# Kernel optimization log

Hardware: AMD Instinct MI355X
Metric: run time of the kernel (lower is better)

## Reference

```python
import jax, jax.numpy as jnp
import numpy as np

N = 100000      # nodes
E = 1600000     # edges (avg degree 16)
D_IN, D_H, D_OUT = 128, 128, 64


def _pow(d, e):
    # torch code zeroes out inf from 0 ** negative_exponent
    p = jnp.power(d, e)
    return jnp.where(jnp.isinf(p), jnp.zeros_like(p), p)


def _gso_weights(params, deg, row, col):
    # params = [m1, m2, m3, e1, e2, e3, a]
    m1, m2, m3, e1, e2, e3, a = (params[i] for i in range(7))
    d = deg + a                       # self-loop-adjusted degrees, [N]
    pe2 = _pow(d, e2)
    pe3 = _pow(d, e3)
    w_edge = m2 * pe2[row] * pe3[col]                     # off-diagonal GSO entries, [E]
    w_self = m1 * _pow(d, e1) + m2 * pe2 * pe3 + m3       # diagonal GSO entries, [N]
    return w_edge, w_self


def setup_inputs() -> dict:
    key = jax.random.key(0)
    ks = jax.random.split(key, 8)
    x = jax.random.normal(ks[0], (N, D_IN), dtype=jnp.float32)
    edge_index = jax.random.randint(ks[1], (2, E), 0, N, dtype=jnp.int32)
    glorot = lambda k, i, o: jax.random.normal(k, (i, o), dtype=jnp.float32) * np.float32(np.sqrt(2.0 / (i + o)))
    W1 = glorot(ks[2], D_IN, D_H)
    W2 = glorot(ks[3], D_H, D_H)
    W3 = glorot(ks[4], D_H, D_OUT)
    b1 = jnp.zeros((D_H,), jnp.float32)
    b2 = jnp.zeros((D_H,), jnp.float32)
    b3 = jnp.zeros((D_OUT,), jnp.float32)
    # [m1, m2, m3, e1, e2, e3, a]
    gso1_params = jnp.array([0.0, 1.0, 0.0, 0.0, -0.5, -0.5, 1.0], jnp.float32)   # NORMADJ
    gso2_params = jnp.array([0.0, -1.0, 1.0, 0.0, -1.0, 0.0, 0.0], jnp.float32)   # RWLAPLACIAN
    return {"x": x, "edge_index": edge_index, "W1": W1, "b1": b1, "W2": W2,
            "b2": b2, "W3": W3, "b3": b3, "gso1_params": gso1_params,
            "gso2_params": gso2_params}


def reference(x, edge_index, W1, b1, W2, b2, W3, b3, gso1_params, gso2_params):
    row, col = edge_index[0], edge_index[1]
    deg = jax.ops.segment_sum(jnp.ones(row.shape, x.dtype), row, num_segments=N)
    we1, ws1 = _gso_weights(gso1_params, deg, row, col)
    we2, ws2 = _gso_weights(gso2_params, deg, row, col)
    w_edge = we1 + we2   # combined two-GSO edge weights, [E]
    w_self = ws1 + ws2   # combined diagonal (self-loop) weights, [N]

    def conv(h, W, b):
        h = h @ W                                                        # [N, d_out]
        agg = jax.ops.segment_sum(w_edge[:, None] * h[col], row, num_segments=N)
        return agg + w_self[:, None] * h + b

    h = jax.nn.relu(conv(x, W1, b1))
    h = jax.nn.relu(conv(h, W2, b2))   # dropout=0.0 (eval) -> identity
    return conv(h, W3, b3)
```

## Files before the change

### kernel.cpp

```cpp
#include <hip/hip_runtime.h>
#include <hip/hip_fp16.h>
#include <math.h>
#include <type_traits>

typedef _Float16 half8 __attribute__((ext_vector_type(8)));
typedef float floatx4 __attribute__((ext_vector_type(4)));

#define RSHIFT 9
#define AGG_BLOCKS 2048

__global__ __launch_bounds__(256) void hist_conv_kernel(
        const int* __restrict__ row, int E, int* __restrict__ bucketsize,
        const float* __restrict__ W1, const float* __restrict__ W2,
        const float* __restrict__ W3, _Float16* __restrict__ Wt1,
        _Float16* __restrict__ Wt2, _Float16* __restrict__ Wt3, int histBlocks) {
    int tid = threadIdx.x;
    if ((int)blockIdx.x < histBlocks) {
        __shared__ int h[256];
        h[tid] = 0;
        __syncthreads();
        int base = blockIdx.x * 16384;
#pragma unroll
        for (int it = 0; it < 16; ++it) {
            int e0 = base + it * 1024 + tid * 4;
            if (e0 + 3 < E) {
                int4 r4 = *(const int4*)&row[e0];
                atomicAdd(&h[r4.x >> RSHIFT], 1);
                atomicAdd(&h[r4.y >> RSHIFT], 1);
                atomicAdd(&h[r4.z >> RSHIFT], 1);
                atomicAdd(&h[r4.w >> RSHIFT], 1);
            } else {
#pragma unroll
                for (int j = 0; j < 4; ++j)
                    if (e0 + j < E) atomicAdd(&h[row[e0 + j] >> RSHIFT], 1);
            }
        }
        __syncthreads();
        if (h[tid]) atomicAdd(&bucketsize[tid], h[tid]);
    } else {
        int g = ((int)blockIdx.x - histBlocks) * 256 + tid;
        if (g < 16384) {
            int k = g >> 7, n = g & 127;
            Wt1[n * 128 + k] = (_Float16)W1[g];
        } else if (g < 32768) {
            int h2 = g - 16384; int k = h2 >> 7, n = h2 & 127;
            Wt2[n * 128 + k] = (_Float16)W2[h2];
        } else if (g < 40960) {
            int h2 = g - 32768; int k = h2 >> 6, n = h2 & 63;
            Wt3[n * 128 + k] = (_Float16)W3[h2];
        }
    }
}

__global__ void scan_buckets_kernel(const int* __restrict__ bucketsize,
                                    int* __restrict__ bucketbase,
                                    int* __restrict__ rowptr, int N, int E) {
    __shared__ int s[256];
    int tid = threadIdx.x;
    int v = bucketsize[tid];
    s[tid] = v;
    __syncthreads();
    for (int off = 1; off < 256; off <<= 1) {
        int u = (tid >= off) ? s[tid - off] : 0;
        __syncthreads();
        s[tid] += u;
        __syncthreads();
    }
    bucketbase[tid] = s[tid] - v;
    if (tid == 255) bucketbase[256] = s[255];
    if (tid == 0) rowptr[N] = E;
}

__global__ __launch_bounds__(256) void partition_kernel(
        const int* __restrict__ row, const int* __restrict__ col,
        const int* __restrict__ bucketbase, int* __restrict__ gcur,
        int* __restrict__ emid, int E, int NB) {
    __shared__ int scnt[256], sofs[256], gslot[256];
    __shared__ int sdata[4096];
    __shared__ unsigned short sbkt[4096];

    int tid = threadIdx.x;
    int base = blockIdx.x * 4096;
    scnt[tid] = 0;
    __syncthreads();

    int epk[16]; int eb[16]; int eidx[16];
#pragma unroll
    for (int v = 0; v < 4; ++v) {
        int e0 = base + v * 1024 + tid * 4;
        int4 r4, c4;
        bool full = (e0 + 3 < E);
        if (full) {
            r4 = *(const int4*)&row[e0];
            c4 = *(const int4*)&col[e0];
        }
#pragma unroll
        for (int j = 0; j < 4; ++j) {
            int u = v * 4 + j;
            eb[u] = -1;
            int r, c;
            if (full) {
                r = (&r4.x)[j]; c = (&c4.x)[j];
            } else {
                if (e0 + j >= E) continue;
                r = row[e0 + j]; c = col[e0 + j];
            }
            int b = r >> RSHIFT;
            eb[u] = b;
            eidx[u] = atomicAdd(&scnt[b], 1);
            epk[u] = c | ((r & ((1 << RSHIFT) - 1)) << 20);
        }
    }
    __syncthreads();
    sofs[tid] = scnt[tid];
    __syncthreads();
    for (int off = 1; off < 256; off <<= 1) {
        int v = (tid >= off) ? sofs[tid - off] : 0;
        __syncthreads();
        sofs[tid] += v;
        __syncthreads();
    }
    int excl = sofs[tid] - scnt[tid];
    sofs[tid] = excl;
    if (tid < NB && scnt[tid] > 0)
        gslot[tid] = bucketbase[tid] + atomicAdd(&gcur[tid], scnt[tid]);
    __syncthreads();
#pragma unroll
    for (int u = 0; u < 16; ++u) {
        if (eb[u] >= 0) {
            int idx = sofs[eb[u]] + eidx[u];
            sdata[idx] = epk[u];
            sbkt[idx] = (unsigned short)eb[u];
        }
    }
    __syncthreads();
    int cntR = min(4096, E - base);
    for (int i = tid; i < cntR; i += 256) {
        int b = sbkt[i];
        emid[gslot[b] + (i - sofs[b])] = sdata[i];
    }
}

__device__ __forceinline__ float pow_z(float d, float e) {
    float p = powf(d, e);
    return isinf(p) ? 0.0f : p;
}

__device__ __forceinline__ void gso_coeff(float deg, const float* __restrict__ p1,
                                          const float* __restrict__ p2,
                                          float4* cf, float* ws) {
    float m1a = p1[0], m2a = p1[1], m3a = p1[2], e1a = p1[3], e2a = p1[4], e3a = p1[5], aa = p1[6];
    float m1b = p2[0], m2b = p2[1], m3b = p2[2], e1b = p2[3], e2b = p2[4], e3b = p2[5], ab = p2[6];
    float d1 = deg + aa, d2 = deg + ab;
    float pa1 = pow_z(d1, e1a), pa2 = pow_z(d1, e2a), pa3 = pow_z(d1, e3a);
    float pb1 = pow_z(d2, e1b), pb2 = pow_z(d2, e2b), pb3 = pow_z(d2, e3b);
    *cf = make_float4(m2a * pa2, pa3, m2b * pb2, pb3);
    *ws = m1a * pa1 + m2a * pa2 * pa3 + m3a
        + m1b * pb1 + m2b * pb2 * pb3 + m3b;
}

__global__ __launch_bounds__(256) void bucket_deg_kernel(
        const int* __restrict__ bucketbase, const int* __restrict__ emid,
        int* __restrict__ rowptr,
        const float* __restrict__ p1, const float* __restrict__ p2,
        float4* __restrict__ coeff, float* __restrict__ wself, int N) {
    __shared__ int cnt[512];
    __shared__ int ssum[256];
    int b = blockIdx.x;
    int tid = threadIdx.x;
    int row0 = b << RSHIFT;
    int nrows = min(512, N - row0);
    cnt[tid] = 0; cnt[tid + 256] = 0;
    __syncthreads();
    int seg0 = bucketbase[b], seg1 = bucketbase[b + 1];
    for (int i = seg0 + tid; i < seg1; i += 256)
        atomicAdd(&cnt[((unsigned)emid[i]) >> 20], 1);
    __syncthreads();
    int a0 = cnt[2 * tid], a1 = cnt[2 * tid + 1];
    int tsum = a0 + a1;
    ssum[tid] = tsum;
    __syncthreads();
    for (int off = 1; off < 256; off <<= 1) {
        int v = (tid >= off) ? ssum[tid - off] : 0;
        __syncthreads();
        ssum[tid] += v;
        __syncthreads();
    }
    int excl = ssum[tid] - tsum;
    if (2 * tid < nrows) {
        rowptr[row0 + 2 * tid] = seg0 + excl;
        float4 cf; float ws;
        gso_coeff((float)a0, p1, p2, &cf, &ws);
        coeff[row0 + 2 * tid] = cf;
        wself[row0 + 2 * tid] = ws;
    }
    if (2 * tid + 1 < nrows) {
        rowptr[row0 + 2 * tid + 1] = seg0 + excl + a0;
        float4 cf; float ws;
        gso_coeff((float)a1, p1, p2, &cf, &ws);
        coeff[row0 + 2 * tid + 1] = cf;
        wself[row0 + 2 * tid + 1] = ws;
    }
}

__global__ __launch_bounds__(256) void bucket_place_kernel(
        const int* __restrict__ bucketbase, const int* __restrict__ emid,
        const int* __restrict__ rowptr, const float4* __restrict__ coeff,
        int2* __restrict__ epack, int N) {
    __shared__ int lcur[512];
    __shared__ float4 scoef[512];
    int b = blockIdx.x;
    int tid = threadIdx.x;
    int row0 = b << RSHIFT;
    int nrows = min(512, N - row0);
#pragma unroll
    for (int u = 0; u < 2; ++u) {
        int j = tid + u * 256;
        if (j < nrows) {
            lcur[j] = rowptr[row0 + j];
            scoef[j] = coeff[row0 + j];
        }
    }
    __syncthreads();
    int seg0 = bucketbase[b], seg1 = bucketbase[b + 1];
    for (int i = seg0 + tid; i < seg1; i += 256) {
        int v = emid[i];
        int rl = ((unsigned)v) >> 20;
        int c = v & 0xFFFFF;
        float4 cr = scoef[rl];
        float4 cc = coeff[c];
        float w = cr.x * cc.y + cr.z * cc.w;
        int pos = atomicAdd(&lcur[rl], 1);
        epack[pos] = make_int2(c, __float_as_int(w));
    }
}

template<int TN, typename AT>
__global__ __launch_bounds__(256) void gemm_mfma(const AT* __restrict__ A,
        const _Float16* __restrict__ Wt, _Float16* __restrict__ C, int n) {
    constexpr int K = 128;
    constexpr int TM = 128;
    constexpr int LDK = K + 8;
    __shared__ _Float16 As[TM][LDK];
    __shared__ _Float16 Bs[TN][LDK];

    int tid = threadIdx.x;
    int wave = tid >> 6, lane = tid & 63;
    int q = lane >> 4, t = lane & 15;
    int rowbase = blockIdx.x * TM;

    if constexpr (std::is_same<AT, float>::value) {
        for (int i = tid; i < TM * K / 4; i += 256) {
            int r = i >> 5;
            int kc = (i & 31) * 4;
            int rr = rowbase + r;
            float4 v = make_float4(0.f, 0.f, 0.f, 0.f);
            if (rr < n) v = *(const float4*)&A[(size_t)rr * K + kc];
            As[r][kc + 0] = (_Float16)v.x;
            As[r][kc + 1] = (_Float16)v.y;
            As[r][kc + 2] = (_Float16)v.z;
            As[r][kc + 3] = (_Float16)v.w;
        }
    } else {
        for (int i = tid; i < TM * K / 8; i += 256) {
            int r = i >> 4;
            int kc = (i & 15) * 8;
            int rr = rowbase + r;
            uint4 v = make_uint4(0u, 0u, 0u, 0u);
            if (rr < n) v = *(const uint4*)&A[(size_t)rr * K + kc];
            *(uint4*)&As[r][kc] = v;
        }
    }
    for (int i = tid; i < TN * K / 8; i += 256) {
        int nr = i >> 4;
        int kc = (i & 15) * 8;
        *(uint4*)&Bs[nr][kc] = *(const uint4*)&Wt[(size_t)nr * K + kc];
    }
    __syncthreads();

    int m0 = wave * 32;
    floatx4 acc0[TN / 16], acc1[TN / 16];
#pragma unroll
    for (int nt = 0; nt < TN / 16; ++nt) {
        acc0[nt] = (floatx4){0.f, 0.f, 0.f, 0.f};
        acc1[nt] = (floatx4){0.f, 0.f, 0.f, 0.f};
    }

#pragma unroll
    for (int kk = 0; kk < K; kk += 32) {
        half8 a0 = *(const half8*)&As[m0 + t][kk + q * 8];
        half8 a1 = *(const half8*)&As[m0 + 16 + t][kk + q * 8];
#pragma unroll
        for (int nt = 0; nt < TN / 16; ++nt) {
            half8 b = *(const half8*)&Bs[nt * 16 + t][kk + q * 8];
            acc0[nt] = __builtin_amdgcn_mfma_f32_16x16x32_f16(a0, b, acc0[nt], 0, 0, 0);
            acc1[nt] = __builtin_amdgcn_mfma_f32_16x16x32_f16(a1, b, acc1[nt], 0, 0, 0);
        }
    }

#pragma unroll
    for (int nt = 0; nt < TN / 16; ++nt) {
#pragma unroll
        for (int r = 0; r < 4; ++r) {
            int rr0 = rowbase + m0 + q * 4 + r;
            if (rr0 < n) C[(size_t)rr0 * TN + nt * 16 + t] = (_Float16)acc0[nt][r];
            int rr1 = rr0 + 16;
            if (rr1 < n) C[(size_t)rr1 * TN + nt * 16 + t] = (_Float16)acc1[nt][r];
        }
    }
}

__global__ __launch_bounds__(256) void agg128_kernel(const __half2* __restrict__ H,
        const int* __restrict__ rowptr, const int2* __restrict__ epack,
        const float* __restrict__ wself, const float* __restrict__ bias,
        __half2* __restrict__ out, int n) {
    int wid = blockIdx.x * 4 + (threadIdx.x >> 6);
    int nw = gridDim.x * 4;
    int lane = threadIdx.x & 63;
    float2 b = *(const float2*)&bias[2 * lane];
    for (int node = wid; node < n; node += nw) {
        int start = rowptr[node], end = rowptr[node + 1];
        float ws = wself[node];
        float2 hs = __half22float2(H[(size_t)node * 64 + lane]);
        float ax = ws * hs.x, ay = ws * hs.y;
        int e = start;
        for (; e + 16 <= end; e += 16) {
            int2 p[16];
#pragma unroll
            for (int j = 0; j < 16; ++j) p[j] = epack[e + j];
            __half2 hh[16];
#pragma unroll
            for (int j = 0; j < 16; ++j) hh[j] = H[(size_t)p[j].x * 64 + lane];
#pragma unroll
            for (int j = 0; j < 16; ++j) {
                float w = __int_as_float(p[j].y);
                float2 f = __half22float2(hh[j]);
                ax += w * f.x; ay += w * f.y;
            }
        }
        if (e + 8 <= end) {
            int2 p[8];
#pragma unroll
            for (int j = 0; j < 8; ++j) p[j] = epack[e + j];
            __half2 hh[8];
#pragma unroll
            for (int j = 0; j < 8; ++j) hh[j] = H[(size_t)p[j].x * 64 + lane];
#pragma unroll
            for (int j = 0; j < 8; ++j) {
                float w = __int_as_float(p[j].y);
                float2 f = __half22float2(hh[j]);
                ax += w * f.x; ay += w * f.y;
            }
            e += 8;
        }
        if (e + 4 <= end) {
            int2 p[4];
#pragma unroll
            for (int j = 0; j < 4; ++j) p[j] = epack[e + j];
            __half2 hh[4];
#pragma unroll
            for (int j = 0; j < 4; ++j) hh[j] = H[(size_t)p[j].x * 64 + lane];
#pragma unroll
            for (int j = 0; j < 4; ++j) {
                float w = __int_as_float(p[j].y);
                float2 f = __half22float2(hh[j]);
                ax += w * f.x; ay += w * f.y;
            }
            e += 4;
        }
        for (; e < end; ++e) {
            int2 pe = epack[e];
            float w = __int_as_float(pe.y);
            float2 f = __half22float2(H[(size_t)pe.x * 64 + lane]);
            ax += w * f.x; ay += w * f.y;
        }
        float vx = fmaxf(ax + b.x, 0.0f);
        float vy = fmaxf(ay + b.y, 0.0f);
        out[(size_t)node * 64 + lane] = __floats2half2_rn(vx, vy);
    }
}

__global__ __launch_bounds__(256) void agg64_kernel(const __half* __restrict__ H,
        const int* __restrict__ rowptr, const int2* __restrict__ epack,
        const float* __restrict__ wself, const float* __restrict__ bias,
        float* __restrict__ out, int n) {
    int wid = blockIdx.x * 4 + (threadIdx.x >> 6);
    int nw = gridDim.x * 4;
    int lane = threadIdx.x & 63;
    float b = bias[lane];
    for (int node = wid; node < n; node += nw) {
        int start = rowptr[node], end = rowptr[node + 1];
        float ws = wself[node];
        float acc = ws * __half2float(H[(size_t)node * 64 + lane]);
        int e = start;
        for (; e + 16 <= end; e += 16) {
            int2 p[16];
#pragma unroll
            for (int j = 0; j < 16; ++j) p[j] = epack[e + j];
            float f[16];
#pragma unroll
            for (int j = 0; j < 16; ++j) f[j] = __half2float(H[(size_t)p[j].x * 64 + lane]);
#pragma unroll
            for (int j = 0; j < 16; ++j) acc += __int_as_float(p[j].y) * f[j];
        }
        if (e + 8 <= end) {
            int2 p[8];
#pragma unroll
            for (int j = 0; j < 8; ++j) p[j] = epack[e + j];
            float f[8];
#pragma unroll
            for (int j = 0; j < 8; ++j) f[j] = __half2float(H[(size_t)p[j].x * 64 + lane]);
#pragma unroll
            for (int j = 0; j < 8; ++j) acc += __int_as_float(p[j].y) * f[j];
            e += 8;
        }
        if (e + 4 <= end) {
            int2 p[4];
#pragma unroll
            for (int j = 0; j < 4; ++j) p[j] = epack[e + j];
            float f[4];
#pragma unroll
            for (int j = 0; j < 4; ++j) f[j] = __half2float(H[(size_t)p[j].x * 64 + lane]);
#pragma unroll
            for (int j = 0; j < 4; ++j) acc += __int_as_float(p[j].y) * f[j];
            e += 4;
        }
        for (; e < end; ++e) {
            int2 pe = epack[e];
            acc += __int_as_float(pe.y) * __half2float(H[(size_t)pe.x * 64 + lane]);
        }
        out[(size_t)node * 64 + lane] = acc + b;
    }
}

extern "C" void kernel_launch(void* const* d_in, const int* in_sizes, int n_in,
                              void* d_out, int out_size, void* d_ws, size_t ws_size,
                              hipStream_t stream) {
    const float* x  = (const float*)d_in[0];
    const int*   ei = (const int*)d_in[1];
    const float* W1 = (const float*)d_in[2];
    const float* b1 = (const float*)d_in[3];
    const float* W2 = (const float*)d_in[4];
    const float* b2 = (const float*)d_in[5];
    const float* W3 = (const float*)d_in[6];
    const float* b3 = (const float*)d_in[7];
    const float* p1 = (const float*)d_in[8];
    const float* p2 = (const float*)d_in[9];

    const int N = in_sizes[0] / 128;
    const int E = in_sizes[1] / 2;
    const int* row = ei;
    const int* col = ei + E;
    const int NB = ((N - 1) >> RSHIFT) + 1;

    char* p = (char*)d_ws;
    auto alloc = [&](size_t bytes) -> void* {
        void* q = (void*)p;
        p += (bytes + 255) & ~(size_t)255;
        return q;
    };
    int*      bucketsize = (int*)alloc(256 * 4);
    int*      gcur       = (int*)alloc(256 * 4);
    int*      bucketbase = (int*)alloc(257 * 4);
    int*      rowptr     = (int*)alloc((size_t)(N + 1) * 4);
    float4*   coeff      = (float4*)alloc((size_t)N * 16);
    float*    wself      = (float*)alloc((size_t)N * 4);
    int*      emid       = (int*)alloc((size_t)E * 4);
    int2*     epack      = (int2*)alloc((size_t)E * 8);
    _Float16* Wt1        = (_Float16*)alloc(128 * 128 * 2);
    _Float16* Wt2        = (_Float16*)alloc(128 * 128 * 2);
    _Float16* Wt3        = (_Float16*)alloc(128 * 64 * 2);
    _Float16* bufH       = (_Float16*)alloc((size_t)N * 128 * 2);
    _Float16* actH       = (_Float16*)alloc((size_t)N * 128 * 2);
    (void)ws_size; (void)n_in;

    hipMemsetAsync(bucketsize, 0, 512 * 4, stream);

    const int histBlocks = (E + 16383) / 16384;
    const int convBlocks = (40960 + 255) / 256;
    hist_conv_kernel<<<histBlocks + convBlocks, 256, 0, stream>>>(
        row, E, bucketsize, W1, W2, W3, Wt1, Wt2, Wt3, histBlocks);
    scan_buckets_kernel<<<1, 256, 0, stream>>>(bucketsize, bucketbase, rowptr, N, E);
    partition_kernel<<<(E + 4095) / 4096, 256, 0, stream>>>(row, col, bucketbase, gcur,
                                                            emid, E, NB);
    bucket_deg_kernel<<<NB, 256, 0, stream>>>(bucketbase, emid, rowptr, p1, p2,
                                              coeff, wself, N);
    bucket_place_kernel<<<NB, 256, 0, stream>>>(bucketbase, emid, rowptr, coeff, epack, N);

    float* out = (float*)d_out;
    int gemmGrid = (N + 127) / 128;
    gemm_mfma<128, float><<<gemmGrid, 256, 0, stream>>>(x, Wt1, bufH, N);
    agg128_kernel<<<AGG_BLOCKS, 256, 0, stream>>>((const __half2*)bufH, rowptr, epack, wself,
                                                  b1, (__half2*)actH, N);
    gemm_mfma<128, _Float16><<<gemmGrid, 256, 0, stream>>>(actH, Wt2, bufH, N);
    agg128_kernel<<<AGG_BLOCKS, 256, 0, stream>>>((const __half2*)bufH, rowptr, epack, wself,
                                                  b2, (__half2*)actH, N);
    gemm_mfma<64, _Float16><<<gemmGrid, 256, 0, stream>>>(actH, Wt3, bufH, N);
    agg64_kernel<<<AGG_BLOCKS, 256, 0, stream>>>((const __half*)bufH, rowptr, epack, wself,
                                                 b3, out, N);
}
```

Baseline: 449.8 us.

## Fold bucket scan into consumer kernels and launch one wavefront per node in aggregation

```diff
diff --git a/kernel.cpp b/kernel.cpp
--- a/kernel.cpp
+++ b/kernel.cpp
@@ -7,7 +7,6 @@
 typedef float floatx4 __attribute__((ext_vector_type(4)));
 
 #define RSHIFT 9
-#define AGG_BLOCKS 2048
 
 __global__ __launch_bounds__(256) void hist_conv_kernel(
         const int* __restrict__ row, int E, int* __restrict__ bucketsize,
@@ -52,38 +51,40 @@
     }
 }
 
-__global__ void scan_buckets_kernel(const int* __restrict__ bucketsize,
-                                    int* __restrict__ bucketbase,
-                                    int* __restrict__ rowptr, int N, int E) {
-    __shared__ int s[256];
-    int tid = threadIdx.x;
-    int v = bucketsize[tid];
-    s[tid] = v;
+__device__ __forceinline__ void scan_bucketsize(const int* __restrict__ bucketsize,
+                                                int* s_incl, int* s_val) {
+    int tid = threadIdx.x & 255;
+    if (threadIdx.x < 256) {
+        int v = bucketsize[tid];
+        s_val[tid] = v;
+        s_incl[tid] = v;
+    }
     __syncthreads();
     for (int off = 1; off < 256; off <<= 1) {
-        int u = (tid >= off) ? s[tid - off] : 0;
-        __syncthreads();
-        s[tid] += u;
-        __syncthreads();
-    }
-    bucketbase[tid] = s[tid] - v;
-    if (tid == 255) bucketbase[256] = s[255];
-    if (tid == 0) rowptr[N] = E;
+        int v = 0;
+        if (threadIdx.x < 256 && tid >= off) v = s_incl[tid - off];
+        __syncthreads();
+        if (threadIdx.x < 256) s_incl[tid] += v;
+        __syncthreads();
+    }
 }
 
 __global__ __launch_bounds__(256) void partition_kernel(
         const int* __restrict__ row, const int* __restrict__ col,
-        const int* __restrict__ bucketbase, int* __restrict__ gcur,
+        const int* __restrict__ bucketsize, int* __restrict__ gcur,
         int* __restrict__ emid, int E, int NB) {
+    __shared__ int sincl[256], sval[256];
     __shared__ int scnt[256], sofs[256], gslot[256];
     __shared__ int sdata[4096];
     __shared__ unsigned short sbkt[4096];
 
     int tid = threadIdx.x;
+    scan_bucketsize(bucketsize, sincl, sval);
+    int mybase = sincl[tid] - sval[tid];
+    scnt[tid] = 0;
+    __syncthreads();
+
     int base = blockIdx.x * 4096;
-    scnt[tid] = 0;
-    __syncthreads();
-
     int epk[16]; int eb[16]; int eidx[16];
 #pragma unroll
     for (int v = 0; v < 4; ++v) {
@@ -123,7 +124,7 @@
     int excl = sofs[tid] - scnt[tid];
     sofs[tid] = excl;
     if (tid < NB && scnt[tid] > 0)
-        gslot[tid] = bucketbase[tid] + atomicAdd(&gcur[tid], scnt[tid]);
+        gslot[tid] = mybase + atomicAdd(&gcur[tid], scnt[tid]);
     __syncthreads();
 #pragma unroll
     for (int u = 0; u < 16; ++u) {
@@ -160,19 +161,22 @@
 }
 
 __global__ __launch_bounds__(256) void bucket_deg_kernel(
-        const int* __restrict__ bucketbase, const int* __restrict__ emid,
+        const int* __restrict__ bucketsize, const int* __restrict__ emid,
         int* __restrict__ rowptr,
         const float* __restrict__ p1, const float* __restrict__ p2,
-        float4* __restrict__ coeff, float* __restrict__ wself, int N) {
+        float4* __restrict__ coeff, float* __restrict__ wself, int N, int NB) {
+    __shared__ int sincl[256], sval[256];
     __shared__ int cnt[512];
     __shared__ int ssum[256];
     int b = blockIdx.x;
     int tid = threadIdx.x;
+    scan_bucketsize(bucketsize, sincl, sval);
+    int seg0 = sincl[b] - sval[b];
+    int seg1 = sincl[b];
     int row0 = b << RSHIFT;
     int nrows = min(512, N - row0);
     cnt[tid] = 0; cnt[tid + 256] = 0;
     __syncthreads();
-    int seg0 = bucketbase[b], seg1 = bucketbase[b + 1];
     for (int i = seg0 + tid; i < seg1; i += 256)
         atomicAdd(&cnt[((unsigned)emid[i]) >> 20], 1);
     __syncthreads();
@@ -201,16 +205,21 @@
         coeff[row0 + 2 * tid + 1] = cf;
         wself[row0 + 2 * tid + 1] = ws;
     }
+    if (tid == 0 && b == NB - 1) rowptr[N] = seg1;
 }
 
 __global__ __launch_bounds__(256) void bucket_place_kernel(
-        const int* __restrict__ bucketbase, const int* __restrict__ emid,
+        const int* __restrict__ bucketsize, const int* __restrict__ emid,
         const int* __restrict__ rowptr, const float4* __restrict__ coeff,
         int2* __restrict__ epack, int N) {
+    __shared__ int sincl[256], sval[256];
     __shared__ int lcur[512];
     __shared__ float4 scoef[512];
     int b = blockIdx.x;
     int tid = threadIdx.x;
+    scan_bucketsize(bucketsize, sincl, sval);
+    int seg0 = sincl[b] - sval[b];
+    int seg1 = sincl[b];
     int row0 = b << RSHIFT;
     int nrows = min(512, N - row0);
 #pragma unroll
@@ -222,7 +231,6 @@
         }
     }
     __syncthreads();
-    int seg0 = bucketbase[b], seg1 = bucketbase[b + 1];
     for (int i = seg0 + tid; i < seg1; i += 256) {
         int v = emid[i];
         int rl = ((unsigned)v) >> 20;
@@ -310,127 +318,122 @@
     }
 }
 
-__global__ __launch_bounds__(256) void agg128_kernel(const __half2* __restrict__ H,
+__global__ __launch_bounds__(1024) void agg128_kernel(const __half2* __restrict__ H,
         const int* __restrict__ rowptr, const int2* __restrict__ epack,
         const float* __restrict__ wself, const float* __restrict__ bias,
         __half2* __restrict__ out, int n) {
-    int wid = blockIdx.x * 4 + (threadIdx.x >> 6);
-    int nw = gridDim.x * 4;
+    int node = blockIdx.x * 16 + (threadIdx.x >> 6);
+    if (node >= n) return;
     int lane = threadIdx.x & 63;
+    int start = rowptr[node], end = rowptr[node + 1];
+    float ws = wself[node];
+    float2 hs = __half22float2(H[(size_t)node * 64 + lane]);
+    float ax = ws * hs.x, ay = ws * hs.y;
+    int e = start;
+    for (; e + 16 <= end; e += 16) {
+        int2 p[16];
+#pragma unroll
+        for (int j = 0; j < 16; ++j) p[j] = epack[e + j];
+        __half2 hh[16];
+#pragma unroll
+        for (int j = 0; j < 16; ++j) hh[j] = H[(size_t)p[j].x * 64 + lane];
+#pragma unroll
+        for (int j = 0; j < 16; ++j) {
+            float w = __int_as_float(p[j].y);
+            float2 f = __half22float2(hh[j]);
+            ax += w * f.x; ay += w * f.y;
+        }
+    }
+    if (e + 8 <= end) {
+        int2 p[8];
+#pragma unroll
+        for (int j = 0; j < 8; ++j) p[j] = epack[e + j];
+        __half2 hh[8];
+#pragma unroll
+        for (int j = 0; j < 8; ++j) hh[j] = H[(size_t)p[j].x * 64 + lane];
+#pragma unroll
+        for (int j = 0; j < 8; ++j) {
+            float w = __int_as_float(p[j].y);
+            float2 f = __half22float2(hh[j]);
+            ax += w * f.x; ay += w * f.y;
+        }
+        e += 8;
+    }
+    if (e + 4 <= end) {
+        int2 p[4];
+#pragma unroll
+        for (int j = 0; j < 4; ++j) p[j] = epack[e + j];
+        __half2 hh[4];
+#pragma unroll
+        for (int j = 0; j < 4; ++j) hh[j] = H[(size_t)p[j].x * 64 + lane];
+#pragma unroll
+        for (int j = 0; j < 4; ++j) {
+            float w = __int_as_float(p[j].y);
+            float2 f = __half22float2(hh[j]);
+            ax += w * f.x; ay += w * f.y;
+        }
+        e += 4;
+    }
+    for (; e < end; ++e) {
+        int2 pe = epack[e];
+        float w = __int_as_float(pe.y);
+        float2 f = __half22float2(H[(size_t)pe.x * 64 + lane]);
+        ax += w * f.x; ay += w * f.y;
+    }
     float2 b = *(const float2*)&bias[2 * lane];
-    for (int node = wid; node < n; node += nw) {
-        int start = rowptr[node], end = rowptr[node + 1];
-        float ws = wself[node];
-        float2 hs = __half22float2(H[(size_t)node * 64 + lane]);
-        float ax = ws * hs.x, ay = ws * hs.y;
-        int e = start;
-        for (; e + 16 <= end; e += 16) {
-            int2 p[16];
-#pragma unroll
-            for (int j = 0; j < 16; ++j) p[j] = epack[e + j];
-            __half2 hh[16];
-#pragma unroll
-            for (int j = 0; j < 16; ++j) hh[j] = H[(size_t)p[j].x * 64 + lane];
-#pragma unroll
-            for (int j = 0; j < 16; ++j) {
-                float w = __int_as_float(p[j].y);
-                float2 f = __half22float2(hh[j]);
-                ax += w * f.x; ay += w * f.y;
-            }
-        }
-        if (e + 8 <= end) {
-            int2 p[8];
-#pragma unroll
-            for (int j = 0; j < 8; ++j) p[j] = epack[e + j];
-            __half2 hh[8];
-#pragma unroll
-            for (int j = 0; j < 8; ++j) hh[j] = H[(size_t)p[j].x * 64 + lane];
-#pragma unroll
-            for (int j = 0; j < 8; ++j) {
-                float w = __int_as_float(p[j].y);
-                float2 f = __half22float2(hh[j]);
-                ax += w * f.x; ay += w * f.y;
-            }
-            e += 8;
-        }
-        if (e + 4 <= end) {
-            int2 p[4];
-#pragma unroll
-            for (int j = 0; j < 4; ++j) p[j] = epack[e + j];
-            __half2 hh[4];
-#pragma unroll
-            for (int j = 0; j < 4; ++j) hh[j] = H[(size_t)p[j].x * 64 + lane];
-#pragma unroll
-            for (int j = 0; j < 4; ++j) {
-                float w = __int_as_float(p[j].y);
-                float2 f = __half22float2(hh[j]);
-                ax += w * f.x; ay += w * f.y;
-            }
-            e += 4;
-        }
-        for (; e < end; ++e) {
-            int2 pe = epack[e];
-            float w = __int_as_float(pe.y);
-            float2 f = __half22float2(H[(size_t)pe.x * 64 + lane]);
-            ax += w * f.x; ay += w * f.y;
-        }
-        float vx = fmaxf(ax + b.x, 0.0f);
-        float vy = fmaxf(ay + b.y, 0.0f);
-        out[(size_t)node * 64 + lane] = __floats2half2_rn(vx, vy);
-    }
-}
-
-__global__ __launch_bounds__(256) void agg64_kernel(const __half* __restrict__ H,
+    float vx = fmaxf(ax + b.x, 0.0f);
+    float vy = fmaxf(ay + b.y, 0.0f);
+    out[(size_t)node * 64 + lane] = __floats2half2_rn(vx, vy);
+}
+
+__global__ __launch_bounds__(1024) void agg64_kernel(const __half* __restrict__ H,
         const int* __restrict__ rowptr, const int2* __restrict__ epack,
         const float* __restrict__ wself, const float* __restrict__ bias,
         float* __restrict__ out, int n) {
-    int wid = blockIdx.x * 4 + (threadIdx.x >> 6);
-    int nw = gridDim.x * 4;
+    int node = blockIdx.x * 16 + (threadIdx.x >> 6);
+    if (node >= n) return;
     int lane = threadIdx.x & 63;
-    float b = bias[lane];
-    for (int node = wid; node < n; node += nw) {
-        int start = rowptr[node], end = rowptr[node + 1];
-        float ws = wself[node];
-        float acc = ws * __half2float(H[(size_t)node * 64 + lane]);
-        int e = start;
-        for (; e + 16 <= end; e += 16) {
-            int2 p[16];
-#pragma unroll
-            for (int j = 0; j < 16; ++j) p[j] = epack[e + j];
-            float f[16];
-#pragma unroll
-            for (int j = 0; j < 16; ++j) f[j] = __half2float(H[(size_t)p[j].x * 64 + lane]);
-#pragma unroll
-            for (int j = 0; j < 16; ++j) acc += __int_as_float(p[j].y) * f[j];
-        }
-        if (e + 8 <= end) {
-            int2 p[8];
-#pragma unroll
-            for (int j = 0; j < 8; ++j) p[j] = epack[e + j];
-            float f[8];
-#pragma unroll
-            for (int j = 0; j < 8; ++j) f[j] = __half2float(H[(size_t)p[j].x * 64 + lane]);
-#pragma unroll
-            for (int j = 0; j < 8; ++j) acc += __int_as_float(p[j].y) * f[j];
-            e += 8;
-        }
-        if (e + 4 <= end) {
-            int2 p[4];
-#pragma unroll
-            for (int j = 0; j < 4; ++j) p[j] = epack[e + j];
-            float f[4];
-#pragma unroll
-            for (int j = 0; j < 4; ++j) f[j] = __half2float(H[(size_t)p[j].x * 64 + lane]);
-#pragma unroll
-            for (int j = 0; j < 4; ++j) acc += __int_as_float(p[j].y) * f[j];
-            e += 4;
-        }
-        for (; e < end; ++e) {
-            int2 pe = epack[e];
-            acc += __int_as_float(pe.y) * __half2float(H[(size_t)pe.x * 64 + lane]);
-        }
-        out[(size_t)node * 64 + lane] = acc + b;
-    }
+    int start = rowptr[node], end = rowptr[node + 1];
+    float ws = wself[node];
+    float acc = ws * __half2float(H[(size_t)node * 64 + lane]);
+    int e = start;
+    for (; e + 16 <= end; e += 16) {
+        int2 p[16];
+#pragma unroll
+        for (int j = 0; j < 16; ++j) p[j] = epack[e + j];
+        float f[16];
+#pragma unroll
+        for (int j = 0; j < 16; ++j) f[j] = __half2float(H[(size_t)p[j].x * 64 + lane]);
+#pragma unroll
+        for (int j = 0; j < 16; ++j) acc += __int_as_float(p[j].y) * f[j];
+    }
+    if (e + 8 <= end) {
+        int2 p[8];
+#pragma unroll
+        for (int j = 0; j < 8; ++j) p[j] = epack[e + j];
+        float f[8];
+#pragma unroll
+        for (int j = 0; j < 8; ++j) f[j] = __half2float(H[(size_t)p[j].x * 64 + lane]);
+#pragma unroll
+        for (int j = 0; j < 8; ++j) acc += __int_as_float(p[j].y) * f[j];
+        e += 8;
+    }
+    if (e + 4 <= end) {
+        int2 p[4];
+#pragma unroll
+        for (int j = 0; j < 4; ++j) p[j] = epack[e + j];
+        float f[4];
+#pragma unroll
+        for (int j = 0; j < 4; ++j) f[j] = __half2float(H[(size_t)p[j].x * 64 + lane]);
+#pragma unroll
+        for (int j = 0; j < 4; ++j) acc += __int_as_float(p[j].y) * f[j];
+        e += 4;
+    }
+    for (; e < end; ++e) {
+        int2 pe = epack[e];
+        acc += __int_as_float(pe.y) * __half2float(H[(size_t)pe.x * 64 + lane]);
+    }
+    out[(size_t)node * 64 + lane] = acc + bias[lane];
 }
 
 extern "C" void kernel_launch(void* const* d_in, const int* in_sizes, int n_in,
@@ -461,7 +464,6 @@
     };
     int*      bucketsize = (int*)alloc(256 * 4);
     int*      gcur       = (int*)alloc(256 * 4);
-    int*      bucketbase = (int*)alloc(257 * 4);
     int*      rowptr     = (int*)alloc((size_t)(N + 1) * 4);
     float4*   coeff      = (float4*)alloc((size_t)N * 16);
     float*    wself      = (float*)alloc((size_t)N * 4);
@@ -480,22 +482,22 @@
     const int convBlocks = (40960 + 255) / 256;
     hist_conv_kernel<<<histBlocks + convBlocks, 256, 0, stream>>>(
         row, E, bucketsize, W1, W2, W3, Wt1, Wt2, Wt3, histBlocks);
-    scan_buckets_kernel<<<1, 256, 0, stream>>>(bucketsize, bucketbase, rowptr, N, E);
-    partition_kernel<<<(E + 4095) / 4096, 256, 0, stream>>>(row, col, bucketbase, gcur,
+    partition_kernel<<<(E + 4095) / 4096, 256, 0, stream>>>(row, col, bucketsize, gcur,
                                                             emid, E, NB);
-    bucket_deg_kernel<<<NB, 256, 0, stream>>>(bucketbase, emid, rowptr, p1, p2,
-                                              coeff, wself, N);
-    bucket_place_kernel<<<NB, 256, 0, stream>>>(bucketbase, emid, rowptr, coeff, epack, N);
+    bucket_deg_kernel<<<NB, 256, 0, stream>>>(bucketsize, emid, rowptr, p1, p2,
+                                              coeff, wself, N, NB);
+    bucket_place_kernel<<<NB, 256, 0, stream>>>(bucketsize, emid, rowptr, coeff, epack, N);
 
     float* out = (float*)d_out;
     int gemmGrid = (N + 127) / 128;
+    int aggGrid = (N + 15) / 16;
     gemm_mfma<128, float><<<gemmGrid, 256, 0, stream>>>(x, Wt1, bufH, N);
-    agg128_kernel<<<AGG_BLOCKS, 256, 0, stream>>>((const __half2*)bufH, rowptr, epack, wself,
-                                                  b1, (__half2*)actH, N);
+    agg128_kernel<<<aggGrid, 1024, 0, stream>>>((const __half2*)bufH, rowptr, epack, wself,
+                                                b1, (__half2*)actH, N);
     gemm_mfma<128, _Float16><<<gemmGrid, 256, 0, stream>>>(actH, Wt2, bufH, N);
-    agg128_kernel<<<AGG_BLOCKS, 256, 0, stream>>>((const __half2*)bufH, rowptr, epack, wself,
-                                                  b2, (__half2*)actH, N);
+    agg128_kernel<<<aggGrid, 1024, 0, stream>>>((const __half2*)bufH, rowptr, epack, wself,
+                                                b2, (__half2*)actH, N);
     gemm_mfma<64, _Float16><<<gemmGrid, 256, 0, stream>>>(actH, Wt3, bufH, N);
-    agg64_kernel<<<AGG_BLOCKS, 256, 0, stream>>>((const __half*)bufH, rowptr, epack, wself,
-                                                 b3, out, N);
-}
+    agg64_kernel<<<aggGrid, 1024, 0, stream>>>((const __half*)bufH, rowptr, epack, wself,
+                                               b3, out, N);
+}
```

Result: slower. 496.1 us (+10.3%).
